# Kernel tuning notes

Measured on AMD Instinct MI355X. Metric: run time of the kernel, lower is better.

Reference implementation:

```python
import jax, jax.numpy as jnp
import numpy as np

D_CONV = 4
D_STATE = 16
DT_RANK = 64


def _silu(x):
    return x * jax.nn.sigmoid(x)


def setup_inputs() -> dict:
    key = jax.random.key(0)
    ks = jax.random.split(key, 10)
    B, L, dim = 2, 1024, 1024
    d_inner = 2 * dim
    s = lambda fan: 1.0 / np.sqrt(fan)
    inp = {
        "x": jax.random.normal(ks[0], (B, L, dim), jnp.float32),
        "ln_w": jnp.ones((dim,), jnp.float32),
        "ln_b": jnp.zeros((dim,), jnp.float32),
        "w_in": jax.random.normal(ks[1], (2 * d_inner, dim), jnp.float32) * s(dim),
        "conv_w": jax.random.normal(ks[2], (d_inner, D_CONV), jnp.float32) * s(D_CONV),
        "conv_b": jnp.zeros((d_inner,), jnp.float32),
        "w_xproj": jax.random.normal(ks[3], (DT_RANK + 2 * D_STATE, d_inner), jnp.float32) * s(d_inner),
        "w_dt": jax.random.normal(ks[4], (d_inner, DT_RANK), jnp.float32) * s(DT_RANK),
        "b_dt": jax.random.normal(ks[5], (d_inner,), jnp.float32) * 0.1,
        # S4D-real init: A = -(1..d_state) per channel
        "a_log": jnp.tile(jnp.log(jnp.arange(1, D_STATE + 1, dtype=jnp.float32)), (d_inner, 1)),
        "d_skip": jnp.ones((d_inner,), jnp.float32),
        "w_out": jax.random.normal(ks[6], (dim, d_inner), jnp.float32) * s(d_inner),
    }
    return inp


def reference(x, ln_w, ln_b, w_in, conv_w, conv_b, w_xproj, w_dt, b_dt, a_log, d_skip, w_out):
    B, L, dim = x.shape
    residual = x

    # LayerNorm
    mu = jnp.mean(x, axis=-1, keepdims=True)
    var = jnp.mean((x - mu) ** 2, axis=-1, keepdims=True)
    xn = (x - mu) * jax.lax.rsqrt(var + 1e-5) * ln_w + ln_b

    # in_proj -> (x_ssm, z) each (B, L, d_inner)
    xz = jnp.einsum("bld,ed->ble", xn, w_in)
    d_inner = xz.shape[-1] // 2
    xs, z = xz[..., :d_inner], xz[..., d_inner:]

    # depthwise causal conv1d (kernel D_CONV) + SiLU
    xp = jnp.pad(xs, ((0, 0), (D_CONV - 1, 0), (0, 0)))
    xc = conv_b
    for k in range(D_CONV):
        xc = xc + conv_w[:, k] * xp[:, k : k + L, :]
    u = _silu(xc)  # (B, L, d_inner)

    # x_proj -> dt, B, C
    x_dbl = jnp.einsum("ble,re->blr", u, w_xproj)
    dt_r = x_dbl[..., :DT_RANK]
    B_ssm = x_dbl[..., DT_RANK : DT_RANK + D_STATE]         # (B, L, n)
    C_ssm = x_dbl[..., DT_RANK + D_STATE :]                 # (B, L, n)

    dt = jax.nn.softplus(jnp.einsum("blr,er->ble", dt_r, w_dt) + b_dt)  # (B, L, d_inner)

    A = -jnp.exp(a_log)  # (d_inner, n)
    deltaA = jnp.exp(jnp.einsum("ble,en->blen", dt, A))            # (B, L, e, n)
    deltaBu = jnp.einsum("ble,bln,ble->blen", dt, B_ssm, u)        # (B, L, e, n)

    # selective scan over L
    def step(h, ins):
        dA_t, dBu_t, C_t = ins
        h = dA_t * h + dBu_t                       # (B, e, n)
        y = jnp.einsum("ben,bn->be", h, C_t)
        return h, y

    h0 = jnp.zeros((B, d_inner, D_STATE), xs.dtype)
    _, ys = jax.lax.scan(
        step,
        h0,
        (deltaA.transpose(1, 0, 2, 3), deltaBu.transpose(1, 0, 2, 3), C_ssm.transpose(1, 0, 2)),
    )
    y = ys.transpose(1, 0, 2) + u * d_skip         # (B, L, e)

    y = y * _silu(z)
    out = jnp.einsum("ble,de->bld", y, w_out)
    return residual + out
```

## Files before the change

kernel.cpp:

```cpp
#include <hip/hip_runtime.h>
#include <hip/hip_bf16.h>


#define LC 16
#define NCHUNK 64

typedef short bf16x8 __attribute__((ext_vector_type(8)));
typedef float f32x4  __attribute__((ext_vector_type(4)));

static __device__ __forceinline__ float siluf(float x) { return x / (1.f + __expf(-x)); }
static __device__ __forceinline__ unsigned short f2bf(float f) {
    unsigned int u = __float_as_uint(f);
    unsigned int r = (u + 0x7fffu + ((u >> 16) & 1u)) >> 16;
    return (unsigned short)r;
}
static __device__ __forceinline__ float bfb(unsigned short u) {
    return __uint_as_float(((unsigned int)u) << 16);
}
static __device__ __forceinline__ void gload_lds16(const void* g, void* l) {
    __builtin_amdgcn_global_load_lds(
        (const __attribute__((address_space(1))) void*)g,
        (__attribute__((address_space(3))) void*)l, 16, 0, 0);
}

__global__ __launch_bounds__(256) void setup_kernel(
    const float* __restrict__ w_in,  unsigned short* __restrict__ w_in_b,
    const float* __restrict__ w_out, unsigned short* __restrict__ w_out_b,
    const float* __restrict__ w_dt,  unsigned short* __restrict__ w_dt_b,
    const float* __restrict__ x,
    const float* __restrict__ ln_w,
    const float* __restrict__ ln_b,
    unsigned short* __restrict__ xn)
{
    int bid = blockIdx.x, tid = threadIdx.x;
    if (bid < 6272) {
        int i = bid * 256 + tid;
        const float* in; unsigned short* outp; int j;
        if (i < 1048576)      { in = w_in;  outp = w_in_b;  j = i; }
        else if (i < 1572864) { in = w_out; outp = w_out_b; j = i - 1048576; }
        else if (i < 1605632) { in = w_dt;  outp = w_dt_b;  j = i - 1572864; }
        else return;
        float4 v = reinterpret_cast<const float4*>(in)[j];
        ushort4 o = { f2bf(v.x), f2bf(v.y), f2bf(v.z), f2bf(v.w) };
        reinterpret_cast<ushort4*>(outp)[j] = o;
        return;
    }
    int m = bid - 6272;
    const float4* xr = reinterpret_cast<const float4*>(x) + (size_t)m * 256;
    float4 r = xr[tid];
    float f0 = r.x, f1 = r.y, f2 = r.z, f3 = r.w;
    float s  = f0 + f1 + f2 + f3;
    float s2 = f0*f0 + f1*f1 + f2*f2 + f3*f3;
    #pragma unroll
    for (int off = 32; off > 0; off >>= 1) {
        s  += __shfl_down(s, off);
        s2 += __shfl_down(s2, off);
    }
    __shared__ float red[8];
    if ((tid & 63) == 0) { red[tid >> 6] = s; red[4 + (tid >> 6)] = s2; }
    __syncthreads();
    float st = red[0] + red[1] + red[2] + red[3];
    float qt = red[4] + red[5] + red[6] + red[7];
    float mu   = st * (1.f / 1024.f);
    float var  = qt * (1.f / 1024.f) - mu * mu;
    float rstd = rsqrtf(var + 1e-5f);
    float4 wv = reinterpret_cast<const float4*>(ln_w)[tid];
    float4 bv = reinterpret_cast<const float4*>(ln_b)[tid];
    ushort4 o = { f2bf((f0 - mu) * rstd * wv.x + bv.x),
                  f2bf((f1 - mu) * rstd * wv.y + bv.y),
                  f2bf((f2 - mu) * rstd * wv.z + bv.z),
                  f2bf((f3 - mu) * rstd * wv.w + bv.w) };
    reinterpret_cast<ushort4*>(xn + (size_t)m * 1024)[tid] = o;
}

__global__ __launch_bounds__(256) void gemm_bf16_nt(
    const unsigned short* __restrict__ A, int lda,
    const unsigned short* __restrict__ B, int ldb,
    int Kslice,
    float* __restrict__ C, unsigned short* __restrict__ Cb, int ldc,
    const float* __restrict__ bias,
    int ep, size_t Cstride)
{
    __shared__ short As[2 * 128 * 32];
    __shared__ short Bs[2 * 64 * 32];
    int tid = threadIdx.x;
    int z = blockIdx.z;
    A += (size_t)z * Kslice;
    B += (size_t)z * Kslice;
    C += (size_t)z * Cstride;
    int m0 = blockIdx.y * 128, n0 = blockIdx.x * 64;
    int lane = tid & 63, wave = tid >> 6;
    int wm = (wave >> 1) * 64, wn = (wave & 1) * 32;
    int frow = lane & 15, fq = lane >> 4;

    f32x4 acc[4][2] = {};

    int lrow = lane >> 2;
    int scol = (lane & 3) * 8;
    const unsigned short* AgL = A + (size_t)(m0 + wave * 32 + lrow) * lda + scol;
    const unsigned short* BgL = B + (size_t)(n0 + wave * 16 + lrow) * ldb + scol;
    int aoff = (wave * 32) * 32;
    int boff = (wave * 16) * 32;

    gload_lds16(AgL,                      As + aoff);
    gload_lds16(AgL + (size_t)16 * lda,   As + aoff + 16 * 32);
    gload_lds16(BgL,                      Bs + boff);

    int cur = 0;
    for (int k0 = 0; k0 < Kslice; k0 += 32) {
        __syncthreads();
        int nk = k0 + 32;
        if (nk < Kslice) {
            int nxt = cur ^ 1;
            gload_lds16(AgL + nk,                     As + nxt * 4096 + aoff);
            gload_lds16(AgL + (size_t)16 * lda + nk,  As + nxt * 4096 + aoff + 16 * 32);
            gload_lds16(BgL + nk,                     Bs + nxt * 2048 + boff);
        }
        const short* Ac = As + cur * 4096;
        const short* Bc = Bs + cur * 2048;
        bf16x8 af[4], bfr[2];
        #pragma unroll
        for (int i = 0; i < 4; ++i)
            af[i] = *reinterpret_cast<const bf16x8*>(Ac + (wm + i * 16 + frow) * 32 + fq * 8);
        #pragma unroll
        for (int j = 0; j < 2; ++j)
            bfr[j] = *reinterpret_cast<const bf16x8*>(Bc + (wn + j * 16 + frow) * 32 + fq * 8);
        #pragma unroll
        for (int i = 0; i < 4; ++i)
            #pragma unroll
            for (int j = 0; j < 2; ++j)
                acc[i][j] = __builtin_amdgcn_mfma_f32_16x16x32_bf16(af[i], bfr[j], acc[i][j], 0, 0, 0);
        cur ^= 1;
    }

    int cn = lane & 15, rq = (lane >> 4) * 4;
    #pragma unroll
    for (int i = 0; i < 4; ++i) {
        #pragma unroll
        for (int j = 0; j < 2; ++j) {
            #pragma unroll
            for (int r = 0; r < 4; ++r) {
                int row = m0 + wm + i * 16 + rq + r;
                int col = n0 + wn + j * 16 + cn;
                float v = acc[i][j][r];
                if (ep == 0) {
                    C[(size_t)row * ldc + col] = v;
                } else if (ep == 1) {
                    v += bias[col];
                    v = (v > 20.f) ? v : log1pf(__expf(v));
                    Cb[(size_t)row * ldc + col] = f2bf(v);
                } else {
                    Cb[(size_t)row * ldc + col] = f2bf(v);
                }
            }
        }
    }
}

__global__ __launch_bounds__(256) void out_reduce(
    const float* __restrict__ part, const float* __restrict__ x,
    float* __restrict__ out)
{
    int i = blockIdx.x * 256 + threadIdx.x;
    float4 s = reinterpret_cast<const float4*>(x)[i];
    #pragma unroll
    for (int z = 0; z < 4; ++z) {
        float4 p = reinterpret_cast<const float4*>(part + (size_t)z * 2097152)[i];
        s.x += p.x; s.y += p.y; s.z += p.z; s.w += p.w;
    }
    reinterpret_cast<float4*>(out)[i] = s;
}

__global__ __launch_bounds__(256) void xproj_splitk(
    const unsigned short* __restrict__ A,
    const float* __restrict__ B,
    float* __restrict__ part)
{
    __shared__ float As[16][68];
    __shared__ float Bs[16][100];
    int tid = threadIdx.x;
    int m0 = blockIdx.x * 64;
    int k0 = blockIdx.y * 128;
    int tx = tid & 15;
    int ty = tid >> 4;
    float acc[4][6] = {};
    int arow = tid >> 2, akg = (tid & 3) << 2;
    int brow1 = (256 + tid) >> 2, bkg1 = ((256 + tid) & 3) << 2;

    for (int ks = 0; ks < 128; ks += 16) {
        ushort4 au = *reinterpret_cast<const ushort4*>(A + (size_t)(m0 + arow) * 2048 + k0 + ks + akg);
        float4 av = make_float4(bfb(au.x), bfb(au.y), bfb(au.z), bfb(au.w));
        float4 bv0 = make_float4(0.f, 0.f, 0.f, 0.f), bv1 = bv0;
        if (arow < 96)  bv0 = *reinterpret_cast<const float4*>(B + (size_t)arow * 2048 + k0 + ks + akg);
        if (brow1 < 96) bv1 = *reinterpret_cast<const float4*>(B + (size_t)brow1 * 2048 + k0 + ks + bkg1);
        __syncthreads();
        As[akg + 0][arow] = av.x; As[akg + 1][arow] = av.y;
        As[akg + 2][arow] = av.z; As[akg + 3][arow] = av.w;
        if (arow < 96) {
            Bs[akg + 0][arow] = bv0.x; Bs[akg + 1][arow] = bv0.y;
            Bs[akg + 2][arow] = bv0.z; Bs[akg + 3][arow] = bv0.w;
        }
        if (brow1 < 96) {
            Bs[bkg1 + 0][brow1] = bv1.x; Bs[bkg1 + 1][brow1] = bv1.y;
            Bs[bkg1 + 2][brow1] = bv1.z; Bs[bkg1 + 3][brow1] = bv1.w;
        }
        __syncthreads();
        #pragma unroll
        for (int k = 0; k < 16; ++k) {
            float aa[4], bb[6];
            #pragma unroll
            for (int i = 0; i < 4; ++i) aa[i] = As[k][ty * 4 + i];
            #pragma unroll
            for (int j = 0; j < 6; ++j) bb[j] = Bs[k][tx * 6 + j];
            #pragma unroll
            for (int i = 0; i < 4; ++i)
                #pragma unroll
                for (int j = 0; j < 6; ++j)
                    acc[i][j] = fmaf(aa[i], bb[j], acc[i][j]);
        }
    }
    float* p = part + (size_t)blockIdx.y * 196608;
    #pragma unroll
    for (int i = 0; i < 4; ++i)
        #pragma unroll
        for (int j = 0; j < 6; ++j)
            p[(size_t)(m0 + ty * 4 + i) * 96 + tx * 6 + j] = acc[i][j];
}

__global__ __launch_bounds__(256) void xproj_reduce(
    const float* __restrict__ part, float* __restrict__ xdbl,
    unsigned short* __restrict__ dtr)
{
    int i = blockIdx.x * 256 + threadIdx.x;
    float s = 0.f;
    #pragma unroll
    for (int sd = 0; sd < 16; ++sd) s += part[(size_t)sd * 196608 + i];
    xdbl[i] = s;
    int m = i / 96, col = i - m * 96;
    if (col < 64) dtr[(size_t)m * 64 + col] = f2bf(s);
}

__global__ __launch_bounds__(256) void conv_silu_kernel(
    const unsigned short* __restrict__ xz,
    const float* __restrict__ cw,
    const float* __restrict__ cb,
    unsigned short* __restrict__ u)
{
    int idx = blockIdx.x * 256 + threadIdx.x;
    int e = idx & 2047;
    int mp = idx >> 11;
    int m0 = mp * 2;
    int l0 = m0 & 1023;
    float r[5];
    #pragma unroll
    for (int k = 0; k < 5; ++k) {
        int lr = l0 - 3 + k;
        r[k] = (lr >= 0) ? bfb(xz[(size_t)(m0 - 3 + k) * 4096 + e]) : 0.f;
    }
    float4 w = *reinterpret_cast<const float4*>(cw + e * 4);
    float base = cb[e];
    float a0 = base + w.x * r[0] + w.y * r[1] + w.z * r[2] + w.w * r[3];
    float a1 = base + w.x * r[1] + w.y * r[2] + w.z * r[3] + w.w * r[4];
    u[(size_t)m0 * 2048 + e]       = f2bf(siluf(a0));
    u[(size_t)(m0 + 1) * 2048 + e] = f2bf(siluf(a1));
}

__global__ __launch_bounds__(256) void scan_part1(
    const unsigned short* __restrict__ dt,
    const unsigned short* __restrict__ u,
    const float* __restrict__ xdbl,
    const float* __restrict__ a_log,
    float* __restrict__ hpart,
    float* __restrict__ Aprod)
{
    int tid = threadIdx.x;
    int ch = tid >> 2, ng = tid & 3;
    int bid = blockIdx.x;
    int c = bid & 63, et = (bid >> 6) & 31, b = bid >> 11;
    int e = et * 64 + ch;
    float4 al = *reinterpret_cast<const float4*>(a_log + e * 16 + ng * 4);
    float A0 = -__expf(al.x), A1 = -__expf(al.y), A2 = -__expf(al.z), A3 = -__expf(al.w);
    size_t rbase = (size_t)b * 1024 + c * LC;
    const unsigned short* dt_p = dt + rbase * 2048 + e;
    const unsigned short* u_p  = u  + rbase * 2048 + e;
    const float* b_p  = xdbl + rbase * 96 + 64 + ng * 4;
    float h0 = 0.f, h1 = 0.f, h2 = 0.f, h3 = 0.f;
    float P0 = 1.f, P1 = 1.f, P2 = 1.f, P3 = 1.f;
    float dt_c = bfb(dt_p[0]);
    float u_c  = bfb(u_p[0]);
    float4 B_c = *reinterpret_cast<const float4*>(b_p);
    #pragma unroll 8
    for (int l = 0; l < LC; ++l) {
        float dt_n = bfb(dt_p[(size_t)(l + 1) * 2048]);
        float u_n  = bfb(u_p[(size_t)(l + 1) * 2048]);
        float4 B_n = *reinterpret_cast<const float4*>(b_p + (size_t)(l + 1) * 96);
        float du = dt_c * u_c;
        float d0 = __expf(dt_c * A0), d1 = __expf(dt_c * A1);
        float d2 = __expf(dt_c * A2), d3 = __expf(dt_c * A3);
        h0 = fmaf(d0, h0, du * B_c.x); P0 *= d0;
        h1 = fmaf(d1, h1, du * B_c.y); P1 *= d1;
        h2 = fmaf(d2, h2, du * B_c.z); P2 *= d2;
        h3 = fmaf(d3, h3, du * B_c.w); P3 *= d3;
        dt_c = dt_n; u_c = u_n; B_c = B_n;
    }
    size_t oidx = (size_t)c * 65536 + ((size_t)b * 2048 + e) * 16 + ng * 4;
    *reinterpret_cast<float4*>(hpart + oidx) = make_float4(h0, h1, h2, h3);
    *reinterpret_cast<float4*>(Aprod + oidx) = make_float4(P0, P1, P2, P3);
}

__global__ __launch_bounds__(256) void scan_combine(
    const float* __restrict__ hpart,
    const float* __restrict__ Aprod,
    float* __restrict__ hinit)
{
    int t = (blockIdx.x * 256 + threadIdx.x) * 4;
    float4 h = make_float4(0.f, 0.f, 0.f, 0.f);
    #pragma unroll
    for (int c = 0; c < NCHUNK; ++c) {
        *reinterpret_cast<float4*>(hinit + (size_t)c * 65536 + t) = h;
        float4 P = *reinterpret_cast<const float4*>(Aprod + (size_t)c * 65536 + t);
        float4 hp = *reinterpret_cast<const float4*>(hpart + (size_t)c * 65536 + t);
        h.x = fmaf(P.x, h.x, hp.x);
        h.y = fmaf(P.y, h.y, hp.y);
        h.z = fmaf(P.z, h.z, hp.z);
        h.w = fmaf(P.w, h.w, hp.w);
    }
}

__global__ __launch_bounds__(256) void scan_part2(
    const unsigned short* __restrict__ dt,
    const unsigned short* __restrict__ u,
    const float* __restrict__ xdbl,
    const unsigned short* __restrict__ xz,
    const float* __restrict__ a_log,
    const float* __restrict__ d_skip,
    const float* __restrict__ hinit,
    unsigned short* __restrict__ y)
{
    int tid = threadIdx.x;
    int ch = tid >> 2, ng = tid & 3;
    int bid = blockIdx.x;
    int c = bid & 63, et = (bid >> 6) & 31, b = bid >> 11;
    int e = et * 64 + ch;
    float4 al = *reinterpret_cast<const float4*>(a_log + e * 16 + ng * 4);
    float A0 = -__expf(al.x), A1 = -__expf(al.y), A2 = -__expf(al.z), A3 = -__expf(al.w);
    float dsk = d_skip[e];
    size_t rbase = (size_t)b * 1024 + c * LC;
    const unsigned short* dt_p = dt + rbase * 2048 + e;
    const unsigned short* u_p  = u  + rbase * 2048 + e;
    const unsigned short* z_p  = xz + rbase * 4096 + 2048 + e;
    const float* bc_p = xdbl + rbase * 96 + 64 + ng * 4;
    unsigned short* y_p = y + rbase * 2048 + e;
    size_t oidx = (size_t)c * 65536 + ((size_t)b * 2048 + e) * 16 + ng * 4;
    float4 hi = *reinterpret_cast<const float4*>(hinit + oidx);
    float h0 = hi.x, h1 = hi.y, h2 = hi.z, h3 = hi.w;
    float dt_c = bfb(dt_p[0]);
    float u_c  = bfb(u_p[0]);
    float4 B_c = *reinterpret_cast<const float4*>(bc_p);
    float4 C_c = *reinterpret_cast<const float4*>(bc_p + 16);
    #pragma unroll 8
    for (int l = 0; l < LC; ++l) {
        float dt_n = bfb(dt_p[(size_t)(l + 1) * 2048]);
        float u_n  = bfb(u_p[(size_t)(l + 1) * 2048]);
        float4 B_n = *reinterpret_cast<const float4*>(bc_p + (size_t)(l + 1) * 96);
        float4 C_n = *reinterpret_cast<const float4*>(bc_p + (size_t)(l + 1) * 96 + 16);
        float du = dt_c * u_c;
        float d0 = __expf(dt_c * A0), d1 = __expf(dt_c * A1);
        float d2 = __expf(dt_c * A2), d3 = __expf(dt_c * A3);
        h0 = fmaf(d0, h0, du * B_c.x);
        h1 = fmaf(d1, h1, du * B_c.y);
        h2 = fmaf(d2, h2, du * B_c.z);
        h3 = fmaf(d3, h3, du * B_c.w);
        float p = h0 * C_c.x + h1 * C_c.y + h2 * C_c.z + h3 * C_c.w;
        p += __shfl_xor(p, 1);
        p += __shfl_xor(p, 2);
        if (ng == 0) {
            float zv = bfb(z_p[(size_t)l * 4096]);
            y_p[(size_t)l * 2048] = f2bf((p + u_c * dsk) * siluf(zv));
        }
        dt_c = dt_n; u_c = u_n; B_c = B_n; C_c = C_n;
    }
}

extern "C" void kernel_launch(void* const* d_in, const int* in_sizes, int n_in,
                              void* d_out, int out_size, void* d_ws, size_t ws_size,
                              hipStream_t stream) {
    const float* x       = (const float*)d_in[0];
    const float* ln_w    = (const float*)d_in[1];
    const float* ln_b    = (const float*)d_in[2];
    const float* w_in    = (const float*)d_in[3];
    const float* conv_w  = (const float*)d_in[4];
    const float* conv_b  = (const float*)d_in[5];
    const float* w_xproj = (const float*)d_in[6];
    const float* w_dt    = (const float*)d_in[7];
    const float* b_dt    = (const float*)d_in[8];
    const float* a_log   = (const float*)d_in[9];
    const float* d_skip  = (const float*)d_in[10];
    const float* w_out   = (const float*)d_in[11];
    float* out = (float*)d_out;

    float* ws = (float*)d_ws;
    unsigned short* xn_b    = (unsigned short*)(ws);
    unsigned short* xz_b    = (unsigned short*)(ws + 1048576);
    unsigned short* u_b     = (unsigned short*)(ws + 5242880);
    float* xdbl  = ws + 7340032;
    unsigned short* dt_b    = (unsigned short*)(ws + 7536640);
    float* hpart = ws + 9633792;
    float* Aprod = ws + 13828096;
    float* hinit = ws + 18022400;
    unsigned short* y_b     = (unsigned short*)(ws + 22216704);
    unsigned short* w_in_b  = (unsigned short*)(ws + 24313856);
    unsigned short* w_out_b = (unsigned short*)(ws + 26411008);
    unsigned short* w_dt_b  = (unsigned short*)(ws + 27459584);
    unsigned short* dtr_b   = (unsigned short*)(ws + 27525120);
    float* xpart = ws + 9633792;
    float* opart = ws + 1048576;

    setup_kernel<<<8320, 256, 0, stream>>>(w_in, w_in_b, w_out, w_out_b, w_dt, w_dt_b,
                                           x, ln_w, ln_b, xn_b);
    gemm_bf16_nt<<<dim3(64, 16, 1), 256, 0, stream>>>(xn_b, 1024, w_in_b, 1024, 1024,
                                                      nullptr, xz_b, 4096, nullptr, 3, 0);
    conv_silu_kernel<<<8192, 256, 0, stream>>>(xz_b, conv_w, conv_b, u_b);
    xproj_splitk<<<dim3(32, 16), 256, 0, stream>>>(u_b, w_xproj, xpart);
    xproj_reduce<<<768, 256, 0, stream>>>(xpart, xdbl, dtr_b);
    gemm_bf16_nt<<<dim3(32, 16, 1), 256, 0, stream>>>(dtr_b, 64, w_dt_b, 64, 64,
                                                      nullptr, dt_b, 2048, b_dt, 1, 0);
    scan_part1<<<4096, 256, 0, stream>>>(dt_b, u_b, xdbl, a_log, hpart, Aprod);
    scan_combine<<<64, 256, 0, stream>>>(hpart, Aprod, hinit);
    scan_part2<<<4096, 256, 0, stream>>>(dt_b, u_b, xdbl, xz_b, a_log, d_skip, hinit, y_b);
    gemm_bf16_nt<<<dim3(16, 16, 4), 256, 0, stream>>>(y_b, 2048, w_out_b, 2048, 512,
                                                      opart, nullptr, 1024, nullptr, 0, 2097152);
    out_reduce<<<2048, 256, 0, stream>>>(opart, x, out);
}
```

Measured before the change: 275.9 us.

## Split-K out_proj via atomics into residual-initialized output; load B fragments directly

The setup kernel now copies the residual x into the output buffer. The out-projection split-K GEMM then accumulates its partial sums into it with atomic adds, which removes the partial-sum buffers and the separate reduce kernel. The GEMM also stops staging the B tile through LDS and loads B fragments straight from global memory into registers, cutting LDS traffic and usage but adding uncoalesced, unpipelined global loads inside the K loop. The atomics make the float summation order nondeterministic.

```diff
diff --git a/kernel.cpp b/kernel.cpp
--- a/kernel.cpp
+++ b/kernel.cpp
@@ -30,7 +30,8 @@
     const float* __restrict__ x,
     const float* __restrict__ ln_w,
     const float* __restrict__ ln_b,
-    unsigned short* __restrict__ xn)
+    unsigned short* __restrict__ xn,
+    float* __restrict__ out)
 {
     int bid = blockIdx.x, tid = threadIdx.x;
     if (bid < 6272) {
@@ -43,6 +44,11 @@
         float4 v = reinterpret_cast<const float4*>(in)[j];
         ushort4 o = { f2bf(v.x), f2bf(v.y), f2bf(v.z), f2bf(v.w) };
         reinterpret_cast<ushort4*>(outp)[j] = o;
+        return;
+    }
+    if (bid >= 8320) {
+        int i = (bid - 8320) * 256 + tid;
+        reinterpret_cast<float4*>(out)[i] = reinterpret_cast<const float4*>(x)[i];
         return;
     }
     int m = bid - 6272;
@@ -82,7 +88,6 @@
     int ep, size_t Cstride)
 {
     __shared__ short As[2 * 128 * 32];
-    __shared__ short Bs[2 * 64 * 32];
     int tid = threadIdx.x;
     int z = blockIdx.z;
     A += (size_t)z * Kslice;
@@ -98,13 +103,11 @@
     int lrow = lane >> 2;
     int scol = (lane & 3) * 8;
     const unsigned short* AgL = A + (size_t)(m0 + wave * 32 + lrow) * lda + scol;
-    const unsigned short* BgL = B + (size_t)(n0 + wave * 16 + lrow) * ldb + scol;
     int aoff = (wave * 32) * 32;
-    int boff = (wave * 16) * 32;
-
-    gload_lds16(AgL,                      As + aoff);
-    gload_lds16(AgL + (size_t)16 * lda,   As + aoff + 16 * 32);
-    gload_lds16(BgL,                      Bs + boff);
+    const unsigned short* Bg = B + (size_t)(n0 + wn + frow) * ldb + fq * 8;
+
+    gload_lds16(AgL,                    As + aoff);
+    gload_lds16(AgL + (size_t)16 * lda, As + aoff + 16 * 32);
 
     int cur = 0;
     for (int k0 = 0; k0 < Kslice; k0 += 32) {
@@ -112,19 +115,18 @@
         int nk = k0 + 32;
         if (nk < Kslice) {
             int nxt = cur ^ 1;
-            gload_lds16(AgL + nk,                     As + nxt * 4096 + aoff);
-            gload_lds16(AgL + (size_t)16 * lda + nk,  As + nxt * 4096 + aoff + 16 * 32);
-            gload_lds16(BgL + nk,                     Bs + nxt * 2048 + boff);
-        }
+            gload_lds16(AgL + nk,                    As + nxt * 4096 + aoff);
+            gload_lds16(AgL + (size_t)16 * lda + nk, As + nxt * 4096 + aoff + 16 * 32);
+        }
+        bf16x8 bfr[2];
+        #pragma unroll
+        for (int j = 0; j < 2; ++j)
+            bfr[j] = *reinterpret_cast<const bf16x8*>(Bg + (size_t)j * 16 * ldb + k0);
         const short* Ac = As + cur * 4096;
-        const short* Bc = Bs + cur * 2048;
-        bf16x8 af[4], bfr[2];
+        bf16x8 af[4];
         #pragma unroll
         for (int i = 0; i < 4; ++i)
             af[i] = *reinterpret_cast<const bf16x8*>(Ac + (wm + i * 16 + frow) * 32 + fq * 8);
-        #pragma unroll
-        for (int j = 0; j < 2; ++j)
-            bfr[j] = *reinterpret_cast<const bf16x8*>(Bc + (wn + j * 16 + frow) * 32 + fq * 8);
         #pragma unroll
         for (int i = 0; i < 4; ++i)
             #pragma unroll
@@ -149,26 +151,14 @@
                     v += bias[col];
                     v = (v > 20.f) ? v : log1pf(__expf(v));
                     Cb[(size_t)row * ldc + col] = f2bf(v);
+                } else if (ep == 2) {
+                    unsafeAtomicAdd(&C[(size_t)row * ldc + col], v);
                 } else {
                     Cb[(size_t)row * ldc + col] = f2bf(v);
                 }
             }
         }
     }
-}
-
-__global__ __launch_bounds__(256) void out_reduce(
-    const float* __restrict__ part, const float* __restrict__ x,
-    float* __restrict__ out)
-{
-    int i = blockIdx.x * 256 + threadIdx.x;
-    float4 s = reinterpret_cast<const float4*>(x)[i];
-    #pragma unroll
-    for (int z = 0; z < 4; ++z) {
-        float4 p = reinterpret_cast<const float4*>(part + (size_t)z * 2097152)[i];
-        s.x += p.x; s.y += p.y; s.z += p.z; s.w += p.w;
-    }
-    reinterpret_cast<float4*>(out)[i] = s;
 }
 
 __global__ __launch_bounds__(256) void xproj_splitk(
@@ -414,10 +404,9 @@
     unsigned short* w_dt_b  = (unsigned short*)(ws + 27459584);
     unsigned short* dtr_b   = (unsigned short*)(ws + 27525120);
     float* xpart = ws + 9633792;
-    float* opart = ws + 1048576;
-
-    setup_kernel<<<8320, 256, 0, stream>>>(w_in, w_in_b, w_out, w_out_b, w_dt, w_dt_b,
-                                           x, ln_w, ln_b, xn_b);
+
+    setup_kernel<<<10368, 256, 0, stream>>>(w_in, w_in_b, w_out, w_out_b, w_dt, w_dt_b,
+                                            x, ln_w, ln_b, xn_b, out);
     gemm_bf16_nt<<<dim3(64, 16, 1), 256, 0, stream>>>(xn_b, 1024, w_in_b, 1024, 1024,
                                                       nullptr, xz_b, 4096, nullptr, 3, 0);
     conv_silu_kernel<<<8192, 256, 0, stream>>>(xz_b, conv_w, conv_b, u_b);
@@ -429,6 +418,5 @@
     scan_combine<<<64, 256, 0, stream>>>(hpart, Aprod, hinit);
     scan_part2<<<4096, 256, 0, stream>>>(dt_b, u_b, xdbl, xz_b, a_log, d_skip, hinit, y_b);
     gemm_bf16_nt<<<dim3(16, 16, 4), 256, 0, stream>>>(y_b, 2048, w_out_b, 2048, 512,
-                                                      opart, nullptr, 1024, nullptr, 0, 2097152);
-    out_reduce<<<2048, 256, 0, stream>>>(opart, x, out);
-}
+                                                      out, nullptr, 1024, nullptr, 2, 0);
+}
```

Measured after the change: 310.8 us. +12.7%, slower.
